# Optimization experiments

Hardware: AMD Instinct MI355X
Metric: run time of the kernel (lower is better)

The kernel has to match this reference:

```python
import jax, jax.numpy as jnp
import numpy as np

EMBED_DIM = 1024
NUM_HEADS = 16
HEAD_DIM = EMBED_DIM // NUM_HEADS
MAX_ORDER = 4
B, T = 4, 1024


def setup_inputs() -> dict:
    key = jax.random.key(0)
    ks = jax.random.split(key, 12)
    s = EMBED_DIM ** -0.5  # ~ torch Linear init scale
    inp = {
        "x": jax.random.normal(ks[0], (B, T, EMBED_DIM), dtype=jnp.float32),
        "noise": jax.random.uniform(ks[1], (B, NUM_HEADS, T, T), dtype=jnp.float32),
        "Wq": jax.random.normal(ks[2], (EMBED_DIM, EMBED_DIM), dtype=jnp.float32) * s,
        "bq": jnp.zeros((EMBED_DIM,), dtype=jnp.float32),
        "Wk": jax.random.normal(ks[3], (EMBED_DIM, EMBED_DIM), dtype=jnp.float32) * s,
        "bk": jnp.zeros((EMBED_DIM,), dtype=jnp.float32),
        "Wv": jax.random.normal(ks[4], (EMBED_DIM, EMBED_DIM), dtype=jnp.float32) * s,
        "bv": jnp.zeros((EMBED_DIM,), dtype=jnp.float32),
        "Wo": jax.random.normal(ks[5], (EMBED_DIM, EMBED_DIM), dtype=jnp.float32) * s,
        "bo": jnp.zeros((EMBED_DIM,), dtype=jnp.float32),
        "theta": jax.random.uniform(ks[6], (NUM_HEADS,), dtype=jnp.float32) * (np.pi / 4),
        "corr_w": jnp.ones((MAX_ORDER + 1,), dtype=jnp.float32) / (MAX_ORDER + 1),
    }
    return inp


def reference(x, noise, Wq, bq, Wk, bk, Wv, bv, Wo, bo, theta, corr_w):
    Bx, Tx, E = x.shape
    H, D = NUM_HEADS, HEAD_DIM
    scale = D ** -0.5

    def proj(W, b):
        y = jnp.einsum("bte,fe->btf", x, W) + b
        return y.reshape(Bx, Tx, H, D).transpose(0, 2, 1, 3)  # [B,H,T,D]

    q = proj(Wq, bq)
    k = proj(Wk, bk)
    v = proj(Wv, bv)

    scores = jnp.einsum("bhtd,bhsd->bhts", q, k) * scale  # [B,H,T,T]

    # theta -> (0, pi/2); per-head scalar angular correction bias
    th = jax.nn.sigmoid(theta) * (jnp.pi / 2)  # [H]
    orders = jnp.arange(1, MAX_ORDER + 1)  # [K]
    ang = 2.0 * orders[:, None].astype(th.dtype) * th[None, :]  # [K,H]
    Qk = jnp.where((orders % 2 == 1)[:, None], jnp.sin(ang), jnp.cos(ang))  # [K,H]
    bias = 0.1 * jnp.einsum("k,kh->h", corr_w[1:], Qk)  # [H]
    scores = scores + bias[None, :, None, None]

    attn = jax.nn.softmax(scores, axis=-1)

    # entropy-based dropout: T = |sin(2*theta)|, keep where noise > mean(T)
    T_mean = jnp.mean(jnp.abs(jnp.sin(2.0 * th)))
    keep = (noise > T_mean).astype(attn.dtype)
    attn = attn * keep / (1.0 - T_mean + 1e-8)

    out = jnp.einsum("bhts,bhsd->bhtd", attn, v)  # [B,H,T,D]
    out = out.transpose(0, 2, 1, 3).reshape(Bx, Tx, E)
    return jnp.einsum("bte,fe->btf", out, Wo) + bo
```

## Files before the change

### kernel.cpp

```cpp
#include <hip/hip_runtime.h>
#include <math.h>


typedef _Float16 f16;
typedef _Float16 f16x8 __attribute__((ext_vector_type(8)));
typedef float    f32x4 __attribute__((ext_vector_type(4)));

constexpr int EMB = 1024;
constexpr int NH  = 16;
constexpr int HD  = 64;
constexpr int NB  = 4;
constexpr int SEQ = 1024;
constexpr int MT  = NB * SEQ;

constexpr size_t WS_SC  = 0;
constexpr size_t WS_XH  = 256;
constexpr size_t SZ_XH  = (size_t)MT * EMB * 2;
constexpr size_t SZ_W   = (size_t)EMB * EMB * 2;
constexpr size_t WS_WQH = WS_XH + SZ_XH;
constexpr size_t WS_WKH = WS_WQH + SZ_W;
constexpr size_t WS_WVH = WS_WKH + SZ_W;
constexpr size_t WS_WOH = WS_WVH + SZ_W;
constexpr size_t SZ_QH  = (size_t)NB * NH * SEQ * HD * 2;
constexpr size_t WS_QH  = WS_WOH + SZ_W;
constexpr size_t WS_KH  = WS_QH + SZ_QH;
constexpr size_t WS_VTH = WS_KH + SZ_QH;
constexpr size_t WS_OA  = WS_VTH + SZ_QH;

#define MFMA16(a,b,c) __builtin_amdgcn_mfma_f32_16x16x32_f16((a),(b),(c),0,0,0)

__global__ void k_setup(const float* __restrict__ theta, float* __restrict__ sc) {
  if (threadIdx.x == 0 && blockIdx.x == 0) {
    double acc = 0.0;
    for (int h = 0; h < NH; ++h) {
      double th = (double)theta[h];
      th = 1.0 / (1.0 + exp(-th)) * (M_PI * 0.5);
      acc += fabs(sin(2.0 * th));
    }
    double tm = acc / (double)NH;
    sc[0] = (float)tm;
    sc[1] = (float)(1.0 / (1.0 - tm + 1e-8));
    ((double*)(sc + 2))[0] = tm;
  }
}

__global__ void k_cvt8(const float* __restrict__ src, f16* __restrict__ dst, int n8) {
  int i = blockIdx.x * blockDim.x + threadIdx.x;
  if (i >= n8) return;
  const float4* s = (const float4*)src + 2 * (size_t)i;
  float4 a = s[0], b = s[1];
  f16x8 o;
  o[0] = (f16)a.x; o[1] = (f16)a.y; o[2] = (f16)a.z; o[3] = (f16)a.w;
  o[4] = (f16)b.x; o[5] = (f16)b.y; o[6] = (f16)b.z; o[7] = (f16)b.w;
  *(f16x8*)(dst + 8 * (size_t)i) = o;
}

template <int OUTMODE>
__global__ __launch_bounds__(256) void k_gemm(
    const f16* __restrict__ A, const f16* __restrict__ Bw,
    const float* __restrict__ bias, void* __restrict__ outp)
{
  __shared__ f16 As[128 * 32];
  __shared__ f16 Bs[128 * 32];
  const int tid  = threadIdx.x;
  const int wave = tid >> 6, lane = tid & 63;
  const int c = lane & 15, g = lane >> 4;
  const int wr = wave >> 1, wc = wave & 1;
  const int bn0 = blockIdx.x * 128;
  const int bm0 = blockIdx.y * 128;

  const int srow = tid >> 2;
  const int scol = (tid & 3) * 8;

  f32x4 acc[4][4];
  #pragma unroll
  for (int i = 0; i < 4; ++i)
    #pragma unroll
    for (int j = 0; j < 4; ++j) acc[i][j] = (f32x4){0.f, 0.f, 0.f, 0.f};

  const f16* Ap = A  + (size_t)bm0 * EMB;
  const f16* Bp = Bw + (size_t)bn0 * EMB;

  for (int k0 = 0; k0 < EMB; k0 += 32) {
    int4 ra0 = *(const int4*)(Ap + (size_t)srow        * EMB + k0 + scol);
    int4 ra1 = *(const int4*)(Ap + (size_t)(srow + 64) * EMB + k0 + scol);
    int4 rb0 = *(const int4*)(Bp + (size_t)srow        * EMB + k0 + scol);
    int4 rb1 = *(const int4*)(Bp + (size_t)(srow + 64) * EMB + k0 + scol);
    __syncthreads();
    *(int4*)(As + srow * 32 + scol)        = ra0;
    *(int4*)(As + (srow + 64) * 32 + scol) = ra1;
    *(int4*)(Bs + srow * 32 + scol)        = rb0;
    *(int4*)(Bs + (srow + 64) * 32 + scol) = rb1;
    __syncthreads();

    f16x8 af[4], bf[4];
    #pragma unroll
    for (int mi = 0; mi < 4; ++mi)
      af[mi] = *(const f16x8*)(As + (wr * 64 + mi * 16 + c) * 32 + g * 8);
    #pragma unroll
    for (int nj = 0; nj < 4; ++nj)
      bf[nj] = *(const f16x8*)(Bs + (wc * 64 + nj * 16 + c) * 32 + g * 8);
    #pragma unroll
    for (int mi = 0; mi < 4; ++mi)
      #pragma unroll
      for (int nj = 0; nj < 4; ++nj)
        acc[mi][nj] = MFMA16(af[mi], bf[nj], acc[mi][nj]);
  }

  #pragma unroll
  for (int mi = 0; mi < 4; ++mi) {
    #pragma unroll
    for (int nj = 0; nj < 4; ++nj) {
      #pragma unroll
      for (int i = 0; i < 4; ++i) {
        int row = bm0 + wr * 64 + mi * 16 + g * 4 + i;
        int col = bn0 + wc * 64 + nj * 16 + c;
        float v = acc[mi][nj][i] + bias[col];
        if (OUTMODE == 2) {
          ((float*)outp)[(size_t)row * EMB + col] = v;
        } else {
          int b = row >> 10, t = row & 1023;
          int h = col >> 6,  d = col & 63;
          size_t idx;
          if (OUTMODE == 0) idx = (((size_t)(b * NH + h)) * SEQ + t) * HD + d;
          else              idx = (((size_t)(b * NH + h)) * HD  + d) * SEQ + t;
          ((f16*)outp)[idx] = (f16)v;
        }
      }
    }
  }
}

__global__ __launch_bounds__(256) void k_attn(
    const f16* __restrict__ Q, const f16* __restrict__ K, const f16* __restrict__ Vt,
    const float* __restrict__ noise, const float* __restrict__ sc,
    f16* __restrict__ Oa)
{
  __shared__ f16 Pl[4][16 * 72];
  const int tid  = threadIdx.x;
  const int wave = tid >> 6, lane = tid & 63;
  const int c = lane & 15, g = lane >> 4;
  const int bh = blockIdx.y;
  const int b  = bh >> 4, h = bh & 15;
  const int q0 = blockIdx.x * 64 + wave * 16;

  const double tmean    = *(const double*)(sc + 2);
  const float inv_cdrop = sc[1];

  const f16* Qp   = Q  + ((size_t)bh * SEQ + q0) * HD;
  const f16* Kp   = K  + (size_t)bh * SEQ * HD;
  const f16* Vp   = Vt + (size_t)bh * HD * SEQ;
  const float* Np = noise + (size_t)bh * SEQ * SEQ;

  f16x8 qa[2];
  qa[0] = *(const f16x8*)(Qp + c * HD + g * 8);
  qa[1] = *(const f16x8*)(Qp + c * HD + 32 + g * 8);

  f32x4 oacc[4];
  #pragma unroll
  for (int n = 0; n < 4; ++n) oacc[n] = (f32x4){0.f, 0.f, 0.f, 0.f};
  float mrun[4], lrun[4];
  #pragma unroll
  for (int i = 0; i < 4; ++i) { mrun[i] = -1e30f; lrun[i] = 0.f; }

  f16* myP = &Pl[wave][0];

  for (int s0 = 0; s0 < SEQ; s0 += 64) {
    f32x4 sa[4];
    #pragma unroll
    for (int n = 0; n < 4; ++n) sa[n] = (f32x4){0.f, 0.f, 0.f, 0.f};
    #pragma unroll
    for (int kc = 0; kc < 2; ++kc) {
      #pragma unroll
      for (int n = 0; n < 4; ++n) {
        f16x8 kb = *(const f16x8*)(Kp + (size_t)(s0 + n * 16 + c) * HD + kc * 32 + g * 8);
        sa[n] = MFMA16(qa[kc], kb, sa[n]);
      }
    }
    #pragma unroll
    for (int n = 0; n < 4; ++n)
      #pragma unroll
      for (int i = 0; i < 4; ++i) sa[n][i] *= 0.125f;

    float rmx[4];
    #pragma unroll
    for (int i = 0; i < 4; ++i)
      rmx[i] = fmaxf(fmaxf(sa[0][i], sa[1][i]), fmaxf(sa[2][i], sa[3][i]));
    #pragma unroll
    for (int off = 1; off < 16; off <<= 1)
      #pragma unroll
      for (int i = 0; i < 4; ++i)
        rmx[i] = fmaxf(rmx[i], __shfl_xor(rmx[i], off, 64));

    float al[4], rs[4];
    #pragma unroll
    for (int i = 0; i < 4; ++i) {
      float mn = fmaxf(mrun[i], rmx[i]);
      al[i] = __expf(mrun[i] - mn);
      mrun[i] = mn;
      rs[i] = 0.f;
    }
    #pragma unroll
    for (int n = 0; n < 4; ++n)
      #pragma unroll
      for (int i = 0; i < 4; ++i) {
        float p = __expf(sa[n][i] - mrun[i]);
        sa[n][i] = p;
        rs[i] += p;
      }
    #pragma unroll
    for (int off = 1; off < 16; off <<= 1)
      #pragma unroll
      for (int i = 0; i < 4; ++i)
        rs[i] += __shfl_xor(rs[i], off, 64);
    #pragma unroll
    for (int i = 0; i < 4; ++i) lrun[i] = lrun[i] * al[i] + rs[i];
    #pragma unroll
    for (int n = 0; n < 4; ++n)
      #pragma unroll
      for (int i = 0; i < 4; ++i) oacc[n][i] *= al[i];

    #pragma unroll
    for (int i = 0; i < 4; ++i) {
      int trow = q0 + g * 4 + i;
      const float* nrow = Np + (size_t)trow * SEQ + s0;
      #pragma unroll
      for (int n = 0; n < 4; ++n) {
        float nz = nrow[n * 16 + c];
        float p  = ((double)nz > tmean) ? sa[n][i] : 0.f;
        myP[(g * 4 + i) * 72 + n * 16 + c] = (f16)p;
      }
    }
    asm volatile("s_waitcnt lgkmcnt(0)" ::: "memory");

    #pragma unroll
    for (int kc = 0; kc < 2; ++kc) {
      f16x8 pa = *(const f16x8*)(myP + c * 72 + kc * 32 + g * 8);
      #pragma unroll
      for (int n = 0; n < 4; ++n) {
        f16x8 vb = *(const f16x8*)(Vp + (size_t)(n * 16 + c) * SEQ + s0 + kc * 32 + g * 8);
        oacc[n] = MFMA16(pa, vb, oacc[n]);
      }
    }
  }

  #pragma unroll
  for (int i = 0; i < 4; ++i) {
    float isc = inv_cdrop / lrun[i];
    int trow = q0 + g * 4 + i;
    f16* orow = Oa + ((size_t)b * SEQ + trow) * EMB + h * HD;
    #pragma unroll
    for (int n = 0; n < 4; ++n)
      orow[n * 16 + c] = (f16)(oacc[n][i] * isc);
  }
}

extern "C" void kernel_launch(void* const* d_in, const int* in_sizes, int n_in,
                              void* d_out, int out_size, void* d_ws, size_t ws_size,
                              hipStream_t stream) {
  const float* x     = (const float*)d_in[0];
  const float* noise = (const float*)d_in[1];
  const float* Wq    = (const float*)d_in[2];
  const float* bq    = (const float*)d_in[3];
  const float* Wk    = (const float*)d_in[4];
  const float* bk    = (const float*)d_in[5];
  const float* Wv    = (const float*)d_in[6];
  const float* bv    = (const float*)d_in[7];
  const float* Wo    = (const float*)d_in[8];
  const float* bo    = (const float*)d_in[9];
  const float* theta = (const float*)d_in[10];

  char* ws = (char*)d_ws;
  float* sc  = (float*)(ws + WS_SC);
  f16* xh    = (f16*)(ws + WS_XH);
  f16* wqh   = (f16*)(ws + WS_WQH);
  f16* wkh   = (f16*)(ws + WS_WKH);
  f16* wvh   = (f16*)(ws + WS_WVH);
  f16* woh   = (f16*)(ws + WS_WOH);
  f16* Qh    = (f16*)(ws + WS_QH);
  f16* Kh    = (f16*)(ws + WS_KH);
  f16* Vth   = (f16*)(ws + WS_VTH);
  f16* Oah   = (f16*)(ws + WS_OA);

  k_setup<<<1, 64, 0, stream>>>(theta, sc);

  k_cvt8<<<(MT * EMB / 8 + 255) / 256, 256, 0, stream>>>(x, xh, MT * EMB / 8);
  k_cvt8<<<(EMB * EMB / 8 + 255) / 256, 256, 0, stream>>>(Wq, wqh, EMB * EMB / 8);
  k_cvt8<<<(EMB * EMB / 8 + 255) / 256, 256, 0, stream>>>(Wk, wkh, EMB * EMB / 8);
  k_cvt8<<<(EMB * EMB / 8 + 255) / 256, 256, 0, stream>>>(Wv, wvh, EMB * EMB / 8);
  k_cvt8<<<(EMB * EMB / 8 + 255) / 256, 256, 0, stream>>>(Wo, woh, EMB * EMB / 8);

  dim3 gemm_grid(EMB / 128, MT / 128);
  k_gemm<0><<<gemm_grid, 256, 0, stream>>>(xh, wqh, bq, (void*)Qh);
  k_gemm<0><<<gemm_grid, 256, 0, stream>>>(xh, wkh, bk, (void*)Kh);
  k_gemm<1><<<gemm_grid, 256, 0, stream>>>(xh, wvh, bv, (void*)Vth);

  k_attn<<<dim3(SEQ / 64, NB * NH), 256, 0, stream>>>(Qh, Kh, Vth, noise, sc, Oah);

  k_gemm<2><<<gemm_grid, 256, 0, stream>>>(Oah, woh, bo, d_out);
}
```

Measured before the change: 590.4 us.

## Precompute dropout bitmask, prefetch K/V tiles, retile GEMMs and batch weight conversion

Adds a kernel that packs the noise>mean comparison into 64-bit keep masks, so attention reads bits instead of fp32 noise. It also folds the 1/8 softmax scale into the Q projection and prefetches K and V tiles into registers. The GEMMs now use 128x64 tiles with padded LDS rows, register prefetch of the next k-slice, and an LDS-transposed vectorized store for V. The four weight conversions are merged into one launch. The mask is a separate pass over the full 256MB noise tensor, and the smaller tiles raise the GEMM block count.

```diff
diff --git a/kernel.cpp b/kernel.cpp
--- a/kernel.cpp
+++ b/kernel.cpp
@@ -5,6 +5,7 @@
 typedef _Float16 f16;
 typedef _Float16 f16x8 __attribute__((ext_vector_type(8)));
 typedef float    f32x4 __attribute__((ext_vector_type(4)));
+typedef unsigned long long u64;
 
 constexpr int EMB = 1024;
 constexpr int NH  = 16;
@@ -18,11 +19,8 @@
 constexpr size_t SZ_XH  = (size_t)MT * EMB * 2;
 constexpr size_t SZ_W   = (size_t)EMB * EMB * 2;
 constexpr size_t WS_WQH = WS_XH + SZ_XH;
-constexpr size_t WS_WKH = WS_WQH + SZ_W;
-constexpr size_t WS_WVH = WS_WKH + SZ_W;
-constexpr size_t WS_WOH = WS_WVH + SZ_W;
 constexpr size_t SZ_QH  = (size_t)NB * NH * SEQ * HD * 2;
-constexpr size_t WS_QH  = WS_WOH + SZ_W;
+constexpr size_t WS_QH  = WS_WQH + 4 * SZ_W;
 constexpr size_t WS_KH  = WS_QH + SZ_QH;
 constexpr size_t WS_VTH = WS_KH + SZ_QH;
 constexpr size_t WS_OA  = WS_VTH + SZ_QH;
@@ -55,76 +53,144 @@
   *(f16x8*)(dst + 8 * (size_t)i) = o;
 }
 
+__global__ void k_cvtW(const float* __restrict__ s0, const float* __restrict__ s1,
+                       const float* __restrict__ s2, const float* __restrict__ s3,
+                       f16* __restrict__ dst) {
+  int i = blockIdx.x * blockDim.x + threadIdx.x;
+  int w   = i >> 17;
+  int off = i & 131071;
+  const float* src = (w == 0) ? s0 : (w == 1) ? s1 : (w == 2) ? s2 : s3;
+  const float4* s = (const float4*)src + 2 * (size_t)off;
+  float4 a = s[0], b = s[1];
+  f16x8 o;
+  o[0] = (f16)a.x; o[1] = (f16)a.y; o[2] = (f16)a.z; o[3] = (f16)a.w;
+  o[4] = (f16)b.x; o[5] = (f16)b.y; o[6] = (f16)b.z; o[7] = (f16)b.w;
+  *(f16x8*)(dst + ((size_t)w << 20) + 8 * (size_t)off) = o;
+}
+
+__global__ __launch_bounds__(256) void k_mask(const float* __restrict__ noise,
+                                              const float* __restrict__ sc,
+                                              u64* __restrict__ mask) {
+  const double tmean = *(const double*)(sc + 2);
+  const int NW = NB * NH * SEQ * (SEQ / 64);
+  int stride = gridDim.x * blockDim.x;
+  for (int w = blockIdx.x * blockDim.x + threadIdx.x; w < NW; w += stride) {
+    const float4* p = (const float4*)(noise + (size_t)w * 64);
+    u64 m = 0;
+    #pragma unroll
+    for (int j = 0; j < 16; ++j) {
+      float4 v = p[j];
+      u64 nib = (u64)(((double)v.x > tmean) ? 1 : 0)
+              | ((u64)(((double)v.y > tmean) ? 1 : 0) << 1)
+              | ((u64)(((double)v.z > tmean) ? 1 : 0) << 2)
+              | ((u64)(((double)v.w > tmean) ? 1 : 0) << 3);
+      m |= nib << (4 * j);
+    }
+    mask[w] = m;
+  }
+}
+
 template <int OUTMODE>
 __global__ __launch_bounds__(256) void k_gemm(
     const f16* __restrict__ A, const f16* __restrict__ Bw,
-    const float* __restrict__ bias, void* __restrict__ outp)
+    const float* __restrict__ bias, float oscale, void* __restrict__ outp)
 {
-  __shared__ f16 As[128 * 32];
-  __shared__ f16 Bs[128 * 32];
+  __shared__ f16 As[128 * 40];
+  __shared__ f16 Bs[64 * 40];
   const int tid  = threadIdx.x;
   const int wave = tid >> 6, lane = tid & 63;
   const int c = lane & 15, g = lane >> 4;
   const int wr = wave >> 1, wc = wave & 1;
-  const int bn0 = blockIdx.x * 128;
+  const int bn0 = blockIdx.x * 64;
   const int bm0 = blockIdx.y * 128;
 
   const int srow = tid >> 2;
   const int scol = (tid & 3) * 8;
 
-  f32x4 acc[4][4];
+  f32x4 acc[4][2];
   #pragma unroll
   for (int i = 0; i < 4; ++i)
     #pragma unroll
-    for (int j = 0; j < 4; ++j) acc[i][j] = (f32x4){0.f, 0.f, 0.f, 0.f};
+    for (int j = 0; j < 2; ++j) acc[i][j] = (f32x4){0.f, 0.f, 0.f, 0.f};
 
   const f16* Ap = A  + (size_t)bm0 * EMB;
   const f16* Bp = Bw + (size_t)bn0 * EMB;
 
+  int4 ra0 = *(const int4*)(Ap + (size_t)srow        * EMB + scol);
+  int4 ra1 = *(const int4*)(Ap + (size_t)(srow + 64) * EMB + scol);
+  int4 rb0 = *(const int4*)(Bp + (size_t)srow        * EMB + scol);
+
   for (int k0 = 0; k0 < EMB; k0 += 32) {
-    int4 ra0 = *(const int4*)(Ap + (size_t)srow        * EMB + k0 + scol);
-    int4 ra1 = *(const int4*)(Ap + (size_t)(srow + 64) * EMB + k0 + scol);
-    int4 rb0 = *(const int4*)(Bp + (size_t)srow        * EMB + k0 + scol);
-    int4 rb1 = *(const int4*)(Bp + (size_t)(srow + 64) * EMB + k0 + scol);
     __syncthreads();
-    *(int4*)(As + srow * 32 + scol)        = ra0;
-    *(int4*)(As + (srow + 64) * 32 + scol) = ra1;
-    *(int4*)(Bs + srow * 32 + scol)        = rb0;
-    *(int4*)(Bs + (srow + 64) * 32 + scol) = rb1;
+    *(int4*)(As + srow * 40 + scol)        = ra0;
+    *(int4*)(As + (srow + 64) * 40 + scol) = ra1;
+    *(int4*)(Bs + srow * 40 + scol)        = rb0;
     __syncthreads();
 
-    f16x8 af[4], bf[4];
+    int k1 = (k0 + 32 < EMB) ? k0 + 32 : k0;
+    ra0 = *(const int4*)(Ap + (size_t)srow        * EMB + k1 + scol);
+    ra1 = *(const int4*)(Ap + (size_t)(srow + 64) * EMB + k1 + scol);
+    rb0 = *(const int4*)(Bp + (size_t)srow        * EMB + k1 + scol);
+
+    f16x8 af[4], bf[2];
     #pragma unroll
     for (int mi = 0; mi < 4; ++mi)
-      af[mi] = *(const f16x8*)(As + (wr * 64 + mi * 16 + c) * 32 + g * 8);
-    #pragma unroll
-    for (int nj = 0; nj < 4; ++nj)
-      bf[nj] = *(const f16x8*)(Bs + (wc * 64 + nj * 16 + c) * 32 + g * 8);
+      af[mi] = *(const f16x8*)(As + (wr * 64 + mi * 16 + c) * 40 + g * 8);
+    #pragma unroll
+    for (int nj = 0; nj < 2; ++nj)
+      bf[nj] = *(const f16x8*)(Bs + (wc * 32 + nj * 16 + c) * 40 + g * 8);
     #pragma unroll
     for (int mi = 0; mi < 4; ++mi)
       #pragma unroll
-      for (int nj = 0; nj < 4; ++nj)
+      for (int nj = 0; nj < 2; ++nj)
         acc[mi][nj] = MFMA16(af[mi], bf[nj], acc[mi][nj]);
   }
 
+  if (OUTMODE == 1) {
+    __syncthreads();
+    f16* T = As + wave * (16 * 36);
+    f16* outh = (f16*)outp;
+    const int f0 = bn0 + wc * 32;
+    const int h  = f0 >> 6;
+    const int dl = lane & 31;
+    const int th = lane >> 5;
+    #pragma unroll
+    for (int mi = 0; mi < 4; ++mi) {
+      #pragma unroll
+      for (int nj = 0; nj < 2; ++nj)
+        #pragma unroll
+        for (int i = 0; i < 4; ++i) {
+          int col = f0 + nj * 16 + c;
+          T[(g * 4 + i) * 36 + nj * 16 + c] = (f16)(acc[mi][nj][i] + bias[col]);
+        }
+      int row0 = bm0 + wr * 64 + mi * 16;
+      int b = row0 >> 10, t0 = (row0 & 1023) + th * 8;
+      f16x8 o;
+      #pragma unroll
+      for (int t = 0; t < 8; ++t) o[t] = T[(th * 8 + t) * 36 + dl];
+      int d = (f0 & 63) + dl - (wc * 32);
+      d = (wc * 32 + dl) & 63;
+      size_t idx = (((size_t)(b * NH + h)) * HD + d) * SEQ + t0;
+      *(f16x8*)(outh + idx) = o;
+    }
+    return;
+  }
+
   #pragma unroll
   for (int mi = 0; mi < 4; ++mi) {
     #pragma unroll
-    for (int nj = 0; nj < 4; ++nj) {
+    for (int nj = 0; nj < 2; ++nj) {
       #pragma unroll
       for (int i = 0; i < 4; ++i) {
         int row = bm0 + wr * 64 + mi * 16 + g * 4 + i;
-        int col = bn0 + wc * 64 + nj * 16 + c;
-        float v = acc[mi][nj][i] + bias[col];
+        int col = bn0 + wc * 32 + nj * 16 + c;
+        float v = (acc[mi][nj][i] + bias[col]) * oscale;
         if (OUTMODE == 2) {
           ((float*)outp)[(size_t)row * EMB + col] = v;
         } else {
           int b = row >> 10, t = row & 1023;
           int h = col >> 6,  d = col & 63;
-          size_t idx;
-          if (OUTMODE == 0) idx = (((size_t)(b * NH + h)) * SEQ + t) * HD + d;
-          else              idx = (((size_t)(b * NH + h)) * HD  + d) * SEQ + t;
-          ((f16*)outp)[idx] = (f16)v;
+          ((f16*)outp)[(((size_t)(b * NH + h)) * SEQ + t) * HD + d] = (f16)v;
         }
       }
     }
@@ -133,7 +199,7 @@
 
 __global__ __launch_bounds__(256) void k_attn(
     const f16* __restrict__ Q, const f16* __restrict__ K, const f16* __restrict__ Vt,
-    const float* __restrict__ noise, const float* __restrict__ sc,
+    const u64* __restrict__ Mask, const float* __restrict__ sc,
     f16* __restrict__ Oa)
 {
   __shared__ f16 Pl[4][16 * 72];
@@ -144,13 +210,12 @@
   const int b  = bh >> 4, h = bh & 15;
   const int q0 = blockIdx.x * 64 + wave * 16;
 
-  const double tmean    = *(const double*)(sc + 2);
   const float inv_cdrop = sc[1];
 
-  const f16* Qp   = Q  + ((size_t)bh * SEQ + q0) * HD;
-  const f16* Kp   = K  + (size_t)bh * SEQ * HD;
-  const f16* Vp   = Vt + (size_t)bh * HD * SEQ;
-  const float* Np = noise + (size_t)bh * SEQ * SEQ;
+  const f16* Qp  = Q  + ((size_t)bh * SEQ + q0) * HD;
+  const f16* Kp  = K  + (size_t)bh * SEQ * HD;
+  const f16* Vp  = Vt + (size_t)bh * HD * SEQ;
+  const u64* Mp  = Mask + (size_t)bh * SEQ * 16;
 
   f16x8 qa[2];
   qa[0] = *(const f16x8*)(Qp + c * HD + g * 8);
@@ -165,22 +230,37 @@
 
   f16* myP = &Pl[wave][0];
 
-  for (int s0 = 0; s0 < SEQ; s0 += 64) {
+  f16x8 kb[8];
+  #pragma unroll
+  for (int kc = 0; kc < 2; ++kc)
+    #pragma unroll
+    for (int n = 0; n < 4; ++n)
+      kb[kc * 4 + n] = *(const f16x8*)(Kp + (size_t)(n * 16 + c) * HD + kc * 32 + g * 8);
+
+  for (int ts = 0; ts < 16; ++ts) {
+    u64 mw[4];
+    #pragma unroll
+    for (int i = 0; i < 4; ++i)
+      mw[i] = Mp[(size_t)(q0 + g * 4 + i) * 16 + ts];
+
     f32x4 sa[4];
     #pragma unroll
     for (int n = 0; n < 4; ++n) sa[n] = (f32x4){0.f, 0.f, 0.f, 0.f};
     #pragma unroll
-    for (int kc = 0; kc < 2; ++kc) {
-      #pragma unroll
-      for (int n = 0; n < 4; ++n) {
-        f16x8 kb = *(const f16x8*)(Kp + (size_t)(s0 + n * 16 + c) * HD + kc * 32 + g * 8);
-        sa[n] = MFMA16(qa[kc], kb, sa[n]);
-      }
-    }
-    #pragma unroll
-    for (int n = 0; n < 4; ++n)
-      #pragma unroll
-      for (int i = 0; i < 4; ++i) sa[n][i] *= 0.125f;
+    for (int kc = 0; kc < 2; ++kc)
+      #pragma unroll
+      for (int n = 0; n < 4; ++n)
+        sa[n] = MFMA16(qa[kc], kb[kc * 4 + n], sa[n]);
+
+    {
+      int tsn = (ts < 15) ? ts + 1 : 15;
+      const f16* Kn = Kp + (size_t)tsn * 64 * HD;
+      #pragma unroll
+      for (int kc = 0; kc < 2; ++kc)
+        #pragma unroll
+        for (int n = 0; n < 4; ++n)
+          kb[kc * 4 + n] = *(const f16x8*)(Kn + (size_t)(n * 16 + c) * HD + kc * 32 + g * 8);
+    }
 
     float rmx[4];
     #pragma unroll
@@ -220,27 +300,27 @@
       #pragma unroll
       for (int i = 0; i < 4; ++i) oacc[n][i] *= al[i];
 
-    #pragma unroll
-    for (int i = 0; i < 4; ++i) {
-      int trow = q0 + g * 4 + i;
-      const float* nrow = Np + (size_t)trow * SEQ + s0;
+    f16x8 vb[8];
+    #pragma unroll
+    for (int kc = 0; kc < 2; ++kc)
+      #pragma unroll
+      for (int n = 0; n < 4; ++n)
+        vb[kc * 4 + n] = *(const f16x8*)(Vp + (size_t)(n * 16 + c) * SEQ + ts * 64 + kc * 32 + g * 8);
+
+    #pragma unroll
+    for (int i = 0; i < 4; ++i)
       #pragma unroll
       for (int n = 0; n < 4; ++n) {
-        float nz = nrow[n * 16 + c];
-        float p  = ((double)nz > tmean) ? sa[n][i] : 0.f;
+        float p = ((mw[i] >> (n * 16 + c)) & 1ULL) ? sa[n][i] : 0.f;
         myP[(g * 4 + i) * 72 + n * 16 + c] = (f16)p;
       }
-    }
-    asm volatile("s_waitcnt lgkmcnt(0)" ::: "memory");
 
     #pragma unroll
     for (int kc = 0; kc < 2; ++kc) {
       f16x8 pa = *(const f16x8*)(myP + c * 72 + kc * 32 + g * 8);
       #pragma unroll
-      for (int n = 0; n < 4; ++n) {
-        f16x8 vb = *(const f16x8*)(Vp + (size_t)(n * 16 + c) * SEQ + s0 + kc * 32 + g * 8);
-        oacc[n] = MFMA16(pa, vb, oacc[n]);
-      }
+      for (int n = 0; n < 4; ++n)
+        oacc[n] = MFMA16(pa, vb[kc * 4 + n], oacc[n]);
     }
   }
 
@@ -273,29 +353,26 @@
   char* ws = (char*)d_ws;
   float* sc  = (float*)(ws + WS_SC);
   f16* xh    = (f16*)(ws + WS_XH);
-  f16* wqh   = (f16*)(ws + WS_WQH);
-  f16* wkh   = (f16*)(ws + WS_WKH);
-  f16* wvh   = (f16*)(ws + WS_WVH);
-  f16* woh   = (f16*)(ws + WS_WOH);
+  f16* wh    = (f16*)(ws + WS_WQH);
   f16* Qh    = (f16*)(ws + WS_QH);
   f16* Kh    = (f16*)(ws + WS_KH);
   f16* Vth   = (f16*)(ws + WS_VTH);
   f16* Oah   = (f16*)(ws + WS_OA);
+  u64* maskw = (u64*)(ws + WS_XH);
 
   k_setup<<<1, 64, 0, stream>>>(theta, sc);
 
-  k_cvt8<<<(MT * EMB / 8 + 255) / 256, 256, 0, stream>>>(x, xh, MT * EMB / 8);
-  k_cvt8<<<(EMB * EMB / 8 + 255) / 256, 256, 0, stream>>>(Wq, wqh, EMB * EMB / 8);
-  k_cvt8<<<(EMB * EMB / 8 + 255) / 256, 256, 0, stream>>>(Wk, wkh, EMB * EMB / 8);
-  k_cvt8<<<(EMB * EMB / 8 + 255) / 256, 256, 0, stream>>>(Wv, wvh, EMB * EMB / 8);
-  k_cvt8<<<(EMB * EMB / 8 + 255) / 256, 256, 0, stream>>>(Wo, woh, EMB * EMB / 8);
-
-  dim3 gemm_grid(EMB / 128, MT / 128);
-  k_gemm<0><<<gemm_grid, 256, 0, stream>>>(xh, wqh, bq, (void*)Qh);
-  k_gemm<0><<<gemm_grid, 256, 0, stream>>>(xh, wkh, bk, (void*)Kh);
-  k_gemm<1><<<gemm_grid, 256, 0, stream>>>(xh, wvh, bv, (void*)Vth);
-
-  k_attn<<<dim3(SEQ / 64, NB * NH), 256, 0, stream>>>(Qh, Kh, Vth, noise, sc, Oah);
-
-  k_gemm<2><<<gemm_grid, 256, 0, stream>>>(Oah, woh, bo, d_out);
-}
+  k_cvt8<<<2048, 256, 0, stream>>>(x, xh, MT * EMB / 8);
+  k_cvtW<<<2048, 256, 0, stream>>>(Wq, Wk, Wv, Wo, wh);
+
+  dim3 gemm_grid(EMB / 64, MT / 128);
+  k_gemm<0><<<gemm_grid, 256, 0, stream>>>(xh, wh,            bq, 0.125f, (void*)Qh);
+  k_gemm<0><<<gemm_grid, 256, 0, stream>>>(xh, wh + (1 << 20), bk, 1.0f,  (void*)Kh);
+  k_gemm<1><<<gemm_grid, 256, 0, stream>>>(xh, wh + (2 << 20), bv, 1.0f,  (void*)Vth);
+
+  k_mask<<<2048, 256, 0, stream>>>(noise, sc, maskw);
+
+  k_attn<<<dim3(SEQ / 64, NB * NH), 256, 0, stream>>>(Qh, Kh, Vth, maskw, sc, Oah);
+
+  k_gemm<2><<<gemm_grid, 256, 0, stream>>>(Oah, wh + (3 << 20), bo, 1.0f, d_out);
+}
```

Measured after the change: 634.0 us. 1.07x slower.
